# Optimization experiments

Hardware: AMD Instinct MI355X
Metric: run time of the kernel (lower is better)

Reference implementation:

```python
import jax, jax.numpy as jnp
import numpy as np

G = 4        # split_group
H = 64       # hidden_size_t = 256 // 4 (causal -> //1)
I = 64       # input_size_t  = 256 // 4
EPS = 1e-5


def _lstm(x, W_ih, W_hh, b):
    """Grouped unidirectional LSTM, PyTorch gate order (i,f,g,o).
    x: (G,B,T,I); W_ih: (G,4H,I); W_hh: (G,4H,H); b: (G,4H) -> (G,B,T,H)"""
    g, bsz, t, _ = x.shape
    h_dim = W_hh.shape[-1]
    # precompute input projections for all timesteps
    xp = jnp.einsum('gbti,gki->gbtk', x, W_ih) + b[:, None, None, :]  # (G,B,T,4H)
    xp = jnp.moveaxis(xp, 2, 0)  # (T,G,B,4H)

    def step(carry, xt):
        h, c = carry
        gates = xt + jnp.einsum('gbh,gkh->gbk', h, W_hh)
        i_g, f_g, g_g, o_g = jnp.split(gates, 4, axis=-1)
        i_g = jax.nn.sigmoid(i_g)
        f_g = jax.nn.sigmoid(f_g)
        g_g = jnp.tanh(g_g)
        o_g = jax.nn.sigmoid(o_g)
        c = f_g * c + i_g * g_g
        h = o_g * jnp.tanh(c)
        return (h, c), h

    h0 = jnp.zeros((g, bsz, h_dim), x.dtype)
    _, hs = jax.lax.scan(step, (h0, h0), xp)  # hs: (T,G,B,H)
    return jnp.moveaxis(hs, 0, 2)  # (G,B,T,H)


def _bn(x, gamma, beta):
    """BatchNorm1d (training stats) over (B,T) per feature. x: (B,T,F)"""
    mean = x.mean(axis=(0, 1))
    var = x.var(axis=(0, 1))
    return (x - mean) * jax.lax.rsqrt(var + EPS) * gamma + beta


def setup_inputs() -> dict:
    key = jax.random.key(0)
    ks = jax.random.split(key, 12)
    s = 0.1
    F = G * H
    return {
        'inpt': jax.random.normal(ks[0], (32, 1000, 256), jnp.float32),
        'W_ih1': jax.random.normal(ks[1], (G, 4 * H, I), jnp.float32) * s,
        'W_hh1': jax.random.normal(ks[2], (G, 4 * H, H), jnp.float32) * s,
        'b1': jax.random.normal(ks[3], (G, 4 * H), jnp.float32) * s,
        'W_ih2': jax.random.normal(ks[4], (G, 4 * H, H), jnp.float32) * s,
        'W_hh2': jax.random.normal(ks[5], (G, 4 * H, H), jnp.float32) * s,
        'b2': jax.random.normal(ks[6], (G, 4 * H), jnp.float32) * s,
        'gamma1': jnp.ones((F,), jnp.float32) + jax.random.normal(ks[7], (F,)) * 0.01,
        'beta1': jax.random.normal(ks[8], (F,), jnp.float32) * 0.01,
        'gamma2': jnp.ones((F,), jnp.float32) + jax.random.normal(ks[9], (F,)) * 0.01,
        'beta2': jax.random.normal(ks[10], (F,), jnp.float32) * 0.01,
    }


def reference(inpt, W_ih1, W_hh1, b1, W_ih2, W_hh2, b2, gamma1, beta1, gamma2, beta2):
    B, T, F = inpt.shape
    # chunk along features -> (G,B,T,I)
    xg = jnp.transpose(inpt.reshape(B, T, G, I), (2, 0, 1, 3))
    y1 = _lstm(xg, W_ih1, W_hh1, b1)  # (G,B,T,H)
    # torch.stack(dim=-1) + flatten: feature index = h*G + g (interleaved)
    x = jnp.transpose(y1, (1, 2, 3, 0)).reshape(B, T, H * G)
    x = _bn(x, gamma1, beta1)
    # chunk again into G contiguous groups of size H
    xg2 = jnp.transpose(x.reshape(B, T, G, H), (2, 0, 1, 3))
    y2 = _lstm(xg2, W_ih2, W_hh2, b2)  # (G,B,T,H)
    # torch.cat(dim=-1): contiguous groups
    x = jnp.transpose(y2, (1, 2, 0, 3)).reshape(B, T, G * H)
    x = _bn(x, gamma2, beta2)
    return x
```

## Files before the change

kernel.cpp:

```cpp
#include <hip/hip_runtime.h>
#include <math.h>

#define G 4
#define H 64
#define T 1000
#define B 32
#define ROWS (B*T)

__device__ __forceinline__ float sigm(float x) {
    return 1.f / (1.f + __expf(-x));
}
__device__ __forceinline__ float tanh_f(float x) {
    return 2.f / (1.f + __expf(-2.f * x)) - 1.f;
}

template<bool BN>
__global__ __launch_bounds__(256)
void xp_proj(const float* __restrict__ xin,
             const float* __restrict__ Wih,
             const float* __restrict__ bias,
             const float* __restrict__ ac,
             float* __restrict__ xp,
             int t0, int tcn, int tcmax, int TT)
{
    int id = blockIdx.x;
    const int tt = id % TT; id /= TT;
    const int b = id & 31;
    const int g = id >> 5;

    __shared__ __align__(16) float xs[64][68];
    __shared__ __align__(16) float ws[64][68];

    const int tx = threadIdx.x & 15, ty = threadIdx.x >> 4;

    #pragma unroll
    for (int j = 0; j < 4; ++j) {
        int idx = j * 1024 + threadIdx.x * 4;
        int r = idx >> 6, ci = idx & 63;
        int tg = t0 + tt * 64 + r; if (tg > T - 1) tg = T - 1;
        float4 v = *(const float4*)&xin[((size_t)b * T + tg) * 256 + g * 64 + ci];
        if (BN) {
            float4 a4 = *(const float4*)&ac[g * 64 + ci];
            float4 c4 = *(const float4*)&ac[256 + g * 64 + ci];
            v.x = fmaf(v.x, a4.x, c4.x);
            v.y = fmaf(v.y, a4.y, c4.y);
            v.z = fmaf(v.z, a4.z, c4.z);
            v.w = fmaf(v.w, a4.w, c4.w);
        }
        *(float4*)&xs[r][ci] = v;
    }

    float* xpb = xp + (size_t)(g * 32 + b) * tcmax * 256;

    for (int kt = 0; kt < 4; ++kt) {
        __syncthreads();
        #pragma unroll
        for (int j = 0; j < 4; ++j) {
            int idx = j * 1024 + threadIdx.x * 4;
            int r = idx >> 6, ci = idx & 63;
            float4 v = *(const float4*)&Wih[(size_t)((g * 256 + kt * 64 + r) << 6) + ci];
            *(float4*)&ws[r][ci] = v;
        }
        __syncthreads();

        float acc[4][4] = {};
        #pragma unroll
        for (int i4 = 0; i4 < 16; ++i4) {
            float4 xv[4], wv[4];
            #pragma unroll
            for (int q = 0; q < 4; ++q) xv[q] = *(const float4*)&xs[ty * 4 + q][i4 * 4];
            #pragma unroll
            for (int q = 0; q < 4; ++q) wv[q] = *(const float4*)&ws[tx * 4 + q][i4 * 4];
            #pragma unroll
            for (int a = 0; a < 4; ++a)
                #pragma unroll
                for (int c = 0; c < 4; ++c) {
                    acc[a][c] = fmaf(xv[a].x, wv[c].x, acc[a][c]);
                    acc[a][c] = fmaf(xv[a].y, wv[c].y, acc[a][c]);
                    acc[a][c] = fmaf(xv[a].z, wv[c].z, acc[a][c]);
                    acc[a][c] = fmaf(xv[a].w, wv[c].w, acc[a][c]);
                }
        }

        const int kbase = kt * 64 + tx * 4;
        const float4 b4 = *(const float4*)&bias[g * 256 + kbase];
        #pragma unroll
        for (int a = 0; a < 4; ++a) {
            int tloc = tt * 64 + ty * 4 + a;
            if (tloc < tcn) {
                float4 o;
                o.x = acc[a][0] + b4.x;
                o.y = acc[a][1] + b4.y;
                o.z = acc[a][2] + b4.z;
                o.w = acc[a][3] + b4.w;
                *(float4*)&xpb[(size_t)tloc * 256 + kbase] = o;
            }
        }
    }
}

template<int LAYER>
__global__ __launch_bounds__(512, 1)
void rec_xp(const float* __restrict__ xp,
            const float* __restrict__ Whh,
            float* __restrict__ out,
            float* __restrict__ stateh, float* __restrict__ statec,
            float* __restrict__ sums,
            int t0, int t1, int tcmax)
{
    const int blk = blockIdx.x;
    const int g = blk >> 5, b = blk & 31;
    const int tid = threadIdx.x;
    const int w = tid >> 6, l = tid & 63;
    const int c8 = l & 7;
    const int jh = (l >> 3) & 1;
    const int gt = l >> 4;
    const int col = w * 8 + c8;
    const int row = gt * 64 + col;

    __shared__ __align__(16) float hsh[2][64];

    float whh[32];
    {
        const float4* wp = (const float4*)&Whh[(size_t)((g * 256 + row) << 6) + jh * 32];
        #pragma unroll
        for (int i = 0; i < 8; ++i) {
            float4 v = wp[i];
            whh[4*i] = v.x; whh[4*i+1] = v.y; whh[4*i+2] = v.z; whh[4*i+3] = v.w;
        }
    }
    const float m  = (gt == 2) ? 2.f : 1.f;
    const float A  = (gt == 2) ? 2.f : 1.f;
    const float Bc = (gt == 2) ? -1.f : 0.f;

    float cst;
    if (t0 == 0) {
        cst = 0.f;
        if (tid < 64) hsh[0][tid] = 0.f;
    } else {
        cst = statec[blk * 64 + col];
        if (tid < 64) hsh[0][tid] = stateh[blk * 64 + tid];
    }

    const float* xpb = xp + (size_t)blk * tcmax * 256 + row;
    float p[4];
    #pragma unroll
    for (int j = 0; j < 4; ++j) {
        int tp = t0 + j; if (tp > t1 - 1) tp = t1 - 1;
        p[j] = xpb[(size_t)(tp - t0) * 256];
    }

    float hl = 0.f, st_s = 0.f, st_ss = 0.f;
    __syncthreads();

    const int nsteps = t1 - t0;
    for (int s4 = 0; s4 < nsteps; s4 += 4) {
        #pragma unroll
        for (int j = 0; j < 4; ++j) {
            const int cur = j & 1;
            float a0 = 0.f, a1 = 0.f, a2 = 0.f, a3 = 0.f;
            const float4* hv = (const float4*)&hsh[cur][jh * 32];
            #pragma unroll
            for (int q = 0; q < 8; ++q) {
                float4 z = hv[q];
                a0 = fmaf(whh[4*q],   z.x, a0);
                a1 = fmaf(whh[4*q+1], z.y, a1);
                a2 = fmaf(whh[4*q+2], z.z, a2);
                a3 = fmaf(whh[4*q+3], z.w, a3);
            }
            float acc = (a0 + a1) + (a2 + a3);
            float full = acc + __shfl_xor(acc, 8);
            float pre = full + p[j];
            {
                int tp = t0 + s4 + j + 4; if (tp > t1 - 1) tp = t1 - 1;
                p[j] = xpb[(size_t)(tp - t0) * 256];
            }
            float act = A / (1.f + __expf(-m * pre)) + Bc;
            float P = act * __shfl_xor(act, 32);
            float Q = __shfl_xor(P, 16);
            cst = fmaf(act, cst, Q);
            float R = __shfl_xor(cst, 32);
            float h = act * tanh_f(R);
            if (gt == 3 && jh == 0) {
                hsh[cur ^ 1][col] = h;
                int t = t0 + s4 + j;
                if (LAYER == 1) out[((size_t)b * T + t) * 256 + col * 4 + g] = h;
                else            out[((size_t)b * T + t) * 256 + g * 64 + col] = h;
                st_s += h;
                st_ss = fmaf(h, h, st_ss);
                hl = h;
            }
            __syncthreads();
        }
    }
    if (gt == 3 && jh == 0) {
        stateh[blk * 64 + col] = hl;
        int f = (LAYER == 1) ? (col * 4 + g) : (g * 64 + col);
        atomicAdd(&sums[f], st_s);
        atomicAdd(&sums[256 + f], st_ss);
    }
    if (gt == 1 && jh == 0) {
        statec[blk * 64 + col] = cst;
    }
}

template<int LAYER>
__global__ __launch_bounds__(256, 1)
void rec_kernel(const float* __restrict__ xin,
                const float* __restrict__ Wih,
                const float* __restrict__ Whh,
                const float* __restrict__ bias,
                const float* __restrict__ bnac,
                float* __restrict__ out)
{
    const int g = blockIdx.x & 3;
    const int b = blockIdx.x >> 2;
    const int k = threadIdx.x;

    __shared__ __align__(16) float xsh[2][64];
    __shared__ __align__(16) float hsh[64];
    __shared__ __align__(16) float gsh[256];

    float wih[64], whh[64];
    {
        const float4* wi = (const float4*)(Wih + (size_t)(g * 256 + k) * 64);
        const float4* wh = (const float4*)(Whh + (size_t)(g * 256 + k) * 64);
        #pragma unroll
        for (int i = 0; i < 16; ++i) {
            float4 v = wi[i];
            wih[4*i] = v.x; wih[4*i+1] = v.y; wih[4*i+2] = v.z; wih[4*i+3] = v.w;
            float4 u = wh[i];
            whh[4*i] = u.x; whh[4*i+1] = u.y; whh[4*i+2] = u.z; whh[4*i+3] = u.w;
        }
    }
    const float bk = bias[g * 256 + k];
    const long rowbase = (long)b * T;
    const int  colbase = g * 64;

    float c = 0.f, af = 1.f, cf = 0.f;
    float xa = 0.f, xb = 0.f;

    if (k < 64) {
        if (LAYER == 2) { af = bnac[colbase + k]; cf = bnac[256 + colbase + k]; }
        hsh[k] = 0.f;
        float x0 = xin[(rowbase + 0) * 256 + colbase + k];
        xsh[0][k] = (LAYER == 2) ? fmaf(x0, af, cf) : x0;
        xa = xin[(rowbase + 1) * 256 + colbase + k];
        xb = xin[(rowbase + 2) * 256 + colbase + k];
    }
    __syncthreads();

    for (int t = 0; t < T; ++t) {
        const int cur = t & 1;
        float xn = 0.f;
        if (k < 64) {
            int tp = t + 3; if (tp > T - 1) tp = T - 1;
            xn = xin[(rowbase + tp) * 256 + colbase + k];
        }
        const float* xs = xsh[cur];
        float a0 = 0.f, a1 = 0.f, a2 = 0.f, a3 = 0.f;
        #pragma unroll
        for (int i = 0; i < 64; i += 4) {
            a0 = fmaf(wih[i],     xs[i],     a0);
            a1 = fmaf(wih[i + 1], xs[i + 1], a1);
            a2 = fmaf(wih[i + 2], xs[i + 2], a2);
            a3 = fmaf(wih[i + 3], xs[i + 3], a3);
        }
        #pragma unroll
        for (int jq = 0; jq < 64; jq += 4) {
            a0 = fmaf(whh[jq],     hsh[jq],     a0);
            a1 = fmaf(whh[jq + 1], hsh[jq + 1], a1);
            a2 = fmaf(whh[jq + 2], hsh[jq + 2], a2);
            a3 = fmaf(whh[jq + 3], hsh[jq + 3], a3);
        }
        const float acc = bk + ((a0 + a1) + (a2 + a3));
        const float act = (k >= 128 && k < 192) ? tanh_f(acc) : sigm(acc);
        gsh[k] = act;
        __syncthreads();

        if (k < 64) {
            const float ig = gsh[k];
            const float fg = gsh[64 + k];
            const float gg = gsh[128 + k];
            const float og = gsh[192 + k];
            c = fmaf(fg, c, ig * gg);
            const float h = og * tanh_f(c);
            hsh[k] = h;
            const long rrow = rowbase + t;
            if (LAYER == 1) out[rrow * 256 + k * 4 + g] = h;
            else            out[rrow * 256 + colbase + k] = h;
            xsh[cur ^ 1][k] = fmaf(xa, af, cf);
            xa = xb; xb = xn;
        }
        __syncthreads();
    }
}

__global__ void zero_ws(float* sums, int n) {
    int i = blockIdx.x * blockDim.x + threadIdx.x;
    if (i < n) sums[i] = 0.f;
}

__global__ __launch_bounds__(256) void stats_reduce(const float* __restrict__ x,
                                                    float* __restrict__ sums)
{
    float s = 0.f, ss = 0.f;
    for (int r = blockIdx.x; r < ROWS; r += gridDim.x) {
        float v = x[(long)r * 256 + threadIdx.x];
        s += v;
        ss = fmaf(v, v, ss);
    }
    atomicAdd(&sums[threadIdx.x], s);
    atomicAdd(&sums[256 + threadIdx.x], ss);
}

__global__ void stats_finalize(const float* __restrict__ sums,
                               const float* __restrict__ gamma,
                               const float* __restrict__ beta,
                               float* __restrict__ ac)
{
    int f = threadIdx.x;
    const float invN = 1.f / (float)ROWS;
    float mean = sums[f] * invN;
    float var  = fmaf(-mean, mean, sums[256 + f] * invN);
    float a = gamma[f] * rsqrtf(var + 1e-5f);
    ac[f]       = a;
    ac[256 + f] = fmaf(-mean, a, beta[f]);
}

__global__ __launch_bounds__(256) void bn_apply(float* __restrict__ x,
                                                const float* __restrict__ ac)
{
    __shared__ float a_s[256], c_s[256];
    a_s[threadIdx.x] = ac[threadIdx.x];
    c_s[threadIdx.x] = ac[256 + threadIdx.x];
    __syncthreads();
    const long n4 = (long)ROWS * 64;
    for (long i = (long)blockIdx.x * blockDim.x + threadIdx.x; i < n4;
         i += (long)gridDim.x * blockDim.x) {
        float4 v = ((float4*)x)[i];
        int f0 = (int)((i * 4) & 255);
        v.x = fmaf(v.x, a_s[f0],     c_s[f0]);
        v.y = fmaf(v.y, a_s[f0 + 1], c_s[f0 + 1]);
        v.z = fmaf(v.z, a_s[f0 + 2], c_s[f0 + 2]);
        v.w = fmaf(v.w, a_s[f0 + 3], c_s[f0 + 3]);
        ((float4*)x)[i] = v;
    }
}

extern "C" void kernel_launch(void* const* d_in, const int* in_sizes, int n_in,
                              void* d_out, int out_size, void* d_ws, size_t ws_size,
                              hipStream_t stream)
{
    const float* inpt   = (const float*)d_in[0];
    const float* Wih1   = (const float*)d_in[1];
    const float* Whh1   = (const float*)d_in[2];
    const float* b1     = (const float*)d_in[3];
    const float* Wih2   = (const float*)d_in[4];
    const float* Whh2   = (const float*)d_in[5];
    const float* b2     = (const float*)d_in[6];
    const float* gamma1 = (const float*)d_in[7];
    const float* beta1  = (const float*)d_in[8];
    const float* gamma2 = (const float*)d_in[9];
    const float* beta2  = (const float*)d_in[10];
    float* out  = (float*)d_out;

    float* sums1 = (float*)d_ws;
    float* sums2 = sums1 + 512;
    float* acbn1 = sums2 + 512;
    float* acbn2 = acbn1 + 512;
    float* sth   = acbn2 + 512;
    float* stc   = sth + 8192;
    float* xpb   = stc + 8192;

    const size_t fixedB = (size_t)(4 * 512 + 2 * 8192) * 4;
    long availT = ((long)ws_size - (long)fixedB) / (128L * 256L * 4L);
    int Tcmax = (availT >= T) ? T : (int)(availT & ~3L);

    if (Tcmax >= 100) {
        zero_ws<<<4, 256, 0, stream>>>(sums1, 1024);

        for (int t0 = 0; t0 < T; t0 += Tcmax) {
            int tcn = T - t0; if (tcn > Tcmax) tcn = Tcmax;
            int TT = (tcn + 63) / 64;
            xp_proj<false><<<128 * TT, 256, 0, stream>>>(
                inpt, Wih1, b1, nullptr, xpb, t0, tcn, Tcmax, TT);
            rec_xp<1><<<128, 512, 0, stream>>>(xpb, Whh1, out, sth, stc, sums1,
                                               t0, t0 + tcn, Tcmax);
        }
        stats_finalize<<<1, 256, 0, stream>>>(sums1, gamma1, beta1, acbn1);

        for (int t0 = 0; t0 < T; t0 += Tcmax) {
            int tcn = T - t0; if (tcn > Tcmax) tcn = Tcmax;
            int TT = (tcn + 63) / 64;
            xp_proj<true><<<128 * TT, 256, 0, stream>>>(
                out, Wih2, b2, acbn1, xpb, t0, tcn, Tcmax, TT);
            rec_xp<2><<<128, 512, 0, stream>>>(xpb, Whh2, out, sth, stc, sums2,
                                               t0, t0 + tcn, Tcmax);
        }
        stats_finalize<<<1, 256, 0, stream>>>(sums2, gamma2, beta2, acbn2);
        bn_apply<<<2048, 256, 0, stream>>>(out, acbn2);
    } else {
        zero_ws<<<2, 256, 0, stream>>>(sums1, 512);
        rec_kernel<1><<<G * B, 256, 0, stream>>>(inpt, Wih1, Whh1, b1, nullptr, out);
        stats_reduce<<<256, 256, 0, stream>>>(out, sums1);
        stats_finalize<<<1, 256, 0, stream>>>(sums1, gamma1, beta1, acbn1);
        rec_kernel<2><<<G * B, 256, 0, stream>>>(out, Wih2, Whh2, b2, acbn1, out);
        zero_ws<<<2, 256, 0, stream>>>(sums2, 512);
        stats_reduce<<<256, 256, 0, stream>>>(out, sums2);
        stats_finalize<<<1, 256, 0, stream>>>(sums2, gamma2, beta2, acbn2);
        bn_apply<<<2048, 256, 0, stream>>>(out, acbn2);
    }
}
```

Baseline: 1.536 ms.

## Overlap input projection with recurrence via double-buffered fused chunk kernels

Splits the time axis into chunks and double-buffers the input-projection workspace, so one fused launch runs the recurrence on the current chunk while extra blocks compute the projection for the next chunk. The recurrent kernel also drops from 512 to 256 threads: each thread now holds a full 64-element W_hh row, which removes the split-K shuffle and simplifies the gate exchange. A lighter workgroup barrier and a raised wave priority are added. The costs are higher register pressure, more sequential FMAs per thread, and projection blocks competing for CUs with the latency-bound recurrence. If the workspace is small the chunks become shorter.

```diff
diff --git a/kernel.cpp b/kernel.cpp
--- a/kernel.cpp
+++ b/kernel.cpp
@@ -14,22 +14,27 @@
     return 2.f / (1.f + __expf(-2.f * x)) - 1.f;
 }
 
+__device__ __forceinline__ void wg_barrier() {
+    asm volatile("s_waitcnt lgkmcnt(0)" ::: "memory");
+    __builtin_amdgcn_s_barrier();
+    __builtin_amdgcn_sched_barrier(0);
+}
+
 template<bool BN>
-__global__ __launch_bounds__(256)
-void xp_proj(const float* __restrict__ xin,
+__device__ __forceinline__ void proj_body(int id,
+             const float* __restrict__ xin,
              const float* __restrict__ Wih,
              const float* __restrict__ bias,
              const float* __restrict__ ac,
              float* __restrict__ xp,
              int t0, int tcn, int tcmax, int TT)
 {
-    int id = blockIdx.x;
     const int tt = id % TT; id /= TT;
     const int b = id & 31;
     const int g = id >> 5;
 
     __shared__ __align__(16) float xs[64][68];
-    __shared__ __align__(16) float ws[64][68];
+    __shared__ __align__(16) float wsm[64][68];
 
     const int tx = threadIdx.x & 15, ty = threadIdx.x >> 4;
 
@@ -59,7 +64,7 @@
             int idx = j * 1024 + threadIdx.x * 4;
             int r = idx >> 6, ci = idx & 63;
             float4 v = *(const float4*)&Wih[(size_t)((g * 256 + kt * 64 + r) << 6) + ci];
-            *(float4*)&ws[r][ci] = v;
+            *(float4*)&wsm[r][ci] = v;
         }
         __syncthreads();
 
@@ -70,7 +75,7 @@
             #pragma unroll
             for (int q = 0; q < 4; ++q) xv[q] = *(const float4*)&xs[ty * 4 + q][i4 * 4];
             #pragma unroll
-            for (int q = 0; q < 4; ++q) wv[q] = *(const float4*)&ws[tx * 4 + q][i4 * 4];
+            for (int q = 0; q < 4; ++q) wv[q] = *(const float4*)&wsm[tx * 4 + q][i4 * 4];
             #pragma unroll
             for (int a = 0; a < 4; ++a)
                 #pragma unroll
@@ -99,32 +104,39 @@
     }
 }
 
+template<bool BN>
+__global__ __launch_bounds__(256)
+void xp_proj(const float* __restrict__ xin, const float* __restrict__ Wih,
+             const float* __restrict__ bias, const float* __restrict__ ac,
+             float* __restrict__ xp, int t0, int tcn, int tcmax, int TT)
+{
+    proj_body<BN>(blockIdx.x, xin, Wih, bias, ac, xp, t0, tcn, tcmax, TT);
+}
+
 template<int LAYER>
-__global__ __launch_bounds__(512, 1)
-void rec_xp(const float* __restrict__ xp,
+__device__ __forceinline__ void rec_body(
+            const float* __restrict__ xp,
             const float* __restrict__ Whh,
             float* __restrict__ out,
             float* __restrict__ stateh, float* __restrict__ statec,
             float* __restrict__ sums,
             int t0, int t1, int tcmax)
 {
+    __builtin_amdgcn_s_setprio(1);
     const int blk = blockIdx.x;
     const int g = blk >> 5, b = blk & 31;
-    const int tid = threadIdx.x;
-    const int w = tid >> 6, l = tid & 63;
-    const int c8 = l & 7;
-    const int jh = (l >> 3) & 1;
-    const int gt = l >> 4;
-    const int col = w * 8 + c8;
+    const int l = threadIdx.x & 63, w = threadIdx.x >> 6;
+    const int c16 = l & 15, gt = l >> 4;
+    const int col = w * 16 + c16;
     const int row = gt * 64 + col;
 
     __shared__ __align__(16) float hsh[2][64];
 
-    float whh[32];
+    float whh[64];
     {
-        const float4* wp = (const float4*)&Whh[(size_t)((g * 256 + row) << 6) + jh * 32];
-        #pragma unroll
-        for (int i = 0; i < 8; ++i) {
+        const float4* wp = (const float4*)&Whh[(size_t)((g * 256 + row) << 6)];
+        #pragma unroll
+        for (int i = 0; i < 16; ++i) {
             float4 v = wp[i];
             whh[4*i] = v.x; whh[4*i+1] = v.y; whh[4*i+2] = v.z; whh[4*i+3] = v.w;
         }
@@ -133,13 +145,12 @@
     const float A  = (gt == 2) ? 2.f : 1.f;
     const float Bc = (gt == 2) ? -1.f : 0.f;
 
-    float cst;
+    float cst = 0.f;
     if (t0 == 0) {
-        cst = 0.f;
-        if (tid < 64) hsh[0][tid] = 0.f;
+        if (threadIdx.x < 64) hsh[0][threadIdx.x] = 0.f;
     } else {
         cst = statec[blk * 64 + col];
-        if (tid < 64) hsh[0][tid] = stateh[blk * 64 + tid];
+        if (threadIdx.x < 64) hsh[0][threadIdx.x] = stateh[blk * 64 + threadIdx.x];
     }
 
     const float* xpb = xp + (size_t)blk * tcmax * 256 + row;
@@ -159,29 +170,27 @@
         for (int j = 0; j < 4; ++j) {
             const int cur = j & 1;
             float a0 = 0.f, a1 = 0.f, a2 = 0.f, a3 = 0.f;
-            const float4* hv = (const float4*)&hsh[cur][jh * 32];
+            const float4* hv = (const float4*)hsh[cur];
             #pragma unroll
-            for (int q = 0; q < 8; ++q) {
+            for (int q = 0; q < 16; ++q) {
                 float4 z = hv[q];
                 a0 = fmaf(whh[4*q],   z.x, a0);
                 a1 = fmaf(whh[4*q+1], z.y, a1);
                 a2 = fmaf(whh[4*q+2], z.z, a2);
                 a3 = fmaf(whh[4*q+3], z.w, a3);
             }
-            float acc = (a0 + a1) + (a2 + a3);
-            float full = acc + __shfl_xor(acc, 8);
-            float pre = full + p[j];
+            float pre = ((a0 + a1) + (a2 + a3)) + p[j];
             {
                 int tp = t0 + s4 + j + 4; if (tp > t1 - 1) tp = t1 - 1;
                 p[j] = xpb[(size_t)(tp - t0) * 256];
             }
             float act = A / (1.f + __expf(-m * pre)) + Bc;
-            float P = act * __shfl_xor(act, 32);
-            float Q = __shfl_xor(P, 16);
-            cst = fmaf(act, cst, Q);
-            float R = __shfl_xor(cst, 32);
-            float h = act * tanh_f(R);
-            if (gt == 3 && jh == 0) {
+            float gg = __shfl_xor(act, 16);
+            float fg = __shfl_xor(act, 32);
+            float ig = __shfl_xor(act, 48);
+            cst = fmaf(fg, cst, ig * gg);
+            float h = act * tanh_f(cst);
+            if (gt == 3) {
                 hsh[cur ^ 1][col] = h;
                 int t = t0 + s4 + j;
                 if (LAYER == 1) out[((size_t)b * T + t) * 256 + col * 4 + g] = h;
@@ -190,17 +199,34 @@
                 st_ss = fmaf(h, h, st_ss);
                 hl = h;
             }
-            __syncthreads();
-        }
-    }
-    if (gt == 3 && jh == 0) {
+            wg_barrier();
+        }
+    }
+    if (gt == 3) {
         stateh[blk * 64 + col] = hl;
+        statec[blk * 64 + col] = cst;
         int f = (LAYER == 1) ? (col * 4 + g) : (g * 64 + col);
         atomicAdd(&sums[f], st_s);
         atomicAdd(&sums[256 + f], st_ss);
     }
-    if (gt == 1 && jh == 0) {
-        statec[blk * 64 + col] = cst;
+}
+
+template<int LAYER, bool PBN>
+__global__ __launch_bounds__(256, 1)
+void fused_step(const float* __restrict__ xpA, const float* __restrict__ Whh,
+                float* __restrict__ out,
+                float* __restrict__ stateh, float* __restrict__ statec,
+                float* __restrict__ sums,
+                int t0, int t1, int tcmax,
+                const float* __restrict__ xin, const float* __restrict__ Wih,
+                const float* __restrict__ bias, const float* __restrict__ acbn,
+                float* __restrict__ xpB, int t0n, int tcnn, int TTn)
+{
+    if (blockIdx.x < 128) {
+        rec_body<LAYER>(xpA, Whh, out, stateh, statec, sums, t0, t1, tcmax);
+    } else {
+        proj_body<PBN>(blockIdx.x - 128, xin, Wih, bias, acbn, xpB,
+                       t0n, tcnn, tcmax, TTn);
     }
 }
 
@@ -374,29 +400,48 @@
     float* xpb   = stc + 8192;
 
     const size_t fixedB = (size_t)(4 * 512 + 2 * 8192) * 4;
-    long availT = ((long)ws_size - (long)fixedB) / (128L * 256L * 4L);
-    int Tcmax = (availT >= T) ? T : (int)(availT & ~3L);
-
-    if (Tcmax >= 100) {
+    const long perT = 128L * 256L * 4L;
+    long availPair = ((long)ws_size - (long)fixedB) / (2L * perT);
+    int Tc = (availPair >= T) ? T : (int)(availPair & ~3L);
+
+    if (Tc >= 8) {
+        float* buf[2] = { xpb, xpb + (size_t)Tc * 128 * 256 };
+        const int nch = (T + Tc - 1) / Tc;
         zero_ws<<<4, 256, 0, stream>>>(sums1, 1024);
 
-        for (int t0 = 0; t0 < T; t0 += Tcmax) {
-            int tcn = T - t0; if (tcn > Tcmax) tcn = Tcmax;
-            int TT = (tcn + 63) / 64;
-            xp_proj<false><<<128 * TT, 256, 0, stream>>>(
-                inpt, Wih1, b1, nullptr, xpb, t0, tcn, Tcmax, TT);
-            rec_xp<1><<<128, 512, 0, stream>>>(xpb, Whh1, out, sth, stc, sums1,
-                                               t0, t0 + tcn, Tcmax);
+        {
+            int tcn0 = (Tc < T) ? Tc : T;
+            int TT0 = (tcn0 + 63) / 64;
+            xp_proj<false><<<128 * TT0, 256, 0, stream>>>(
+                inpt, Wih1, b1, nullptr, buf[0], 0, tcn0, Tc, TT0);
+            for (int c = 0; c < nch; ++c) {
+                int t0 = c * Tc;
+                int t1 = t0 + Tc; if (t1 > T) t1 = T;
+                int t0n = t1;
+                int tcnn = (c + 1 < nch) ? ((T - t0n < Tc) ? (T - t0n) : Tc) : 0;
+                int TTn = (tcnn + 63) / 64;
+                fused_step<1, false><<<128 + 128 * TTn, 256, 0, stream>>>(
+                    buf[c & 1], Whh1, out, sth, stc, sums1, t0, t1, Tc,
+                    inpt, Wih1, b1, nullptr, buf[(c + 1) & 1], t0n, tcnn, TTn);
+            }
         }
         stats_finalize<<<1, 256, 0, stream>>>(sums1, gamma1, beta1, acbn1);
 
-        for (int t0 = 0; t0 < T; t0 += Tcmax) {
-            int tcn = T - t0; if (tcn > Tcmax) tcn = Tcmax;
-            int TT = (tcn + 63) / 64;
-            xp_proj<true><<<128 * TT, 256, 0, stream>>>(
-                out, Wih2, b2, acbn1, xpb, t0, tcn, Tcmax, TT);
-            rec_xp<2><<<128, 512, 0, stream>>>(xpb, Whh2, out, sth, stc, sums2,
-                                               t0, t0 + tcn, Tcmax);
+        {
+            int tcn0 = (Tc < T) ? Tc : T;
+            int TT0 = (tcn0 + 63) / 64;
+            xp_proj<true><<<128 * TT0, 256, 0, stream>>>(
+                out, Wih2, b2, acbn1, buf[0], 0, tcn0, Tc, TT0);
+            for (int c = 0; c < nch; ++c) {
+                int t0 = c * Tc;
+                int t1 = t0 + Tc; if (t1 > T) t1 = T;
+                int t0n = t1;
+                int tcnn = (c + 1 < nch) ? ((T - t0n < Tc) ? (T - t0n) : Tc) : 0;
+                int TTn = (tcnn + 63) / 64;
+                fused_step<2, true><<<128 + 128 * TTn, 256, 0, stream>>>(
+                    buf[c & 1], Whh2, out, sth, stc, sums2, t0, t1, Tc,
+                    out, Wih2, b2, acbn1, buf[(c + 1) & 1], t0n, tcnn, TTn);
+            }
         }
         stats_finalize<<<1, 256, 0, stream>>>(sums2, gamma2, beta2, acbn2);
         bn_apply<<<2048, 256, 0, stream>>>(out, acbn2);
```

New measurement: 1.583 ms. 1.03x slower.

## Pack two sequences per block with all-four-gate threads in recurrent kernel

Applied to the files above, without the earlier changes.

The recurrent LSTM kernel now runs two (group,batch) sequences per 512-thread block, using 256 threads per sequence. Each thread holds all four gate rows for one hidden column over a 16-wide k slice and reduces across lanes with two xor shuffles. This removes the cross-gate shuffles and halves the number of blocks. The plain __syncthreads is replaced by a custom barrier that waits on LDS and sets wave priority. The cost is longer per-thread FMA chains and the two sequences stepping in lockstep under one barrier.

```diff
diff --git a/kernel.cpp b/kernel.cpp
--- a/kernel.cpp
+++ b/kernel.cpp
@@ -12,6 +12,12 @@
 }
 __device__ __forceinline__ float tanh_f(float x) {
     return 2.f / (1.f + __expf(-2.f * x)) - 1.f;
+}
+
+__device__ __forceinline__ void wg_barrier() {
+    asm volatile("s_waitcnt lgkmcnt(0)" ::: "memory");
+    __builtin_amdgcn_s_barrier();
+    __builtin_amdgcn_sched_barrier(0);
 }
 
 template<bool BN>
@@ -29,7 +35,7 @@
     const int g = id >> 5;
 
     __shared__ __align__(16) float xs[64][68];
-    __shared__ __align__(16) float ws[64][68];
+    __shared__ __align__(16) float wsm[64][68];
 
     const int tx = threadIdx.x & 15, ty = threadIdx.x >> 4;
 
@@ -59,7 +65,7 @@
             int idx = j * 1024 + threadIdx.x * 4;
             int r = idx >> 6, ci = idx & 63;
             float4 v = *(const float4*)&Wih[(size_t)((g * 256 + kt * 64 + r) << 6) + ci];
-            *(float4*)&ws[r][ci] = v;
+            *(float4*)&wsm[r][ci] = v;
         }
         __syncthreads();
 
@@ -70,7 +76,7 @@
             #pragma unroll
             for (int q = 0; q < 4; ++q) xv[q] = *(const float4*)&xs[ty * 4 + q][i4 * 4];
             #pragma unroll
-            for (int q = 0; q < 4; ++q) wv[q] = *(const float4*)&ws[tx * 4 + q][i4 * 4];
+            for (int q = 0; q < 4; ++q) wv[q] = *(const float4*)&wsm[tx * 4 + q][i4 * 4];
             #pragma unroll
             for (int a = 0; a < 4; ++a)
                 #pragma unroll
@@ -101,53 +107,52 @@
 
 template<int LAYER>
 __global__ __launch_bounds__(512, 1)
-void rec_xp(const float* __restrict__ xp,
-            const float* __restrict__ Whh,
-            float* __restrict__ out,
-            float* __restrict__ stateh, float* __restrict__ statec,
-            float* __restrict__ sums,
-            int t0, int t1, int tcmax)
-{
-    const int blk = blockIdx.x;
+void rec2(const float* __restrict__ xp,
+          const float* __restrict__ Whh,
+          float* __restrict__ out,
+          float* __restrict__ stateh, float* __restrict__ statec,
+          float* __restrict__ sums,
+          int t0, int t1, int tcmax)
+{
+    __builtin_amdgcn_s_setprio(1);
+    const int seq = threadIdx.x >> 8;
+    const int tid = threadIdx.x & 255;
+    const int blk = blockIdx.x * 2 + seq;
     const int g = blk >> 5, b = blk & 31;
-    const int tid = threadIdx.x;
     const int w = tid >> 6, l = tid & 63;
-    const int c8 = l & 7;
-    const int jh = (l >> 3) & 1;
-    const int gt = l >> 4;
-    const int col = w * 8 + c8;
-    const int row = gt * 64 + col;
-
-    __shared__ __align__(16) float hsh[2][64];
-
-    float whh[32];
-    {
-        const float4* wp = (const float4*)&Whh[(size_t)((g * 256 + row) << 6) + jh * 32];
-        #pragma unroll
-        for (int i = 0; i < 8; ++i) {
-            float4 v = wp[i];
-            whh[4*i] = v.x; whh[4*i+1] = v.y; whh[4*i+2] = v.z; whh[4*i+3] = v.w;
-        }
-    }
-    const float m  = (gt == 2) ? 2.f : 1.f;
-    const float A  = (gt == 2) ? 2.f : 1.f;
-    const float Bc = (gt == 2) ? -1.f : 0.f;
-
-    float cst;
+    const int c16 = l & 15, ks = l >> 4;
+    const int col = w * 16 + c16;
+
+    __shared__ __align__(16) float hsh[2][2][64];
+
+    float whh[4][16];
+    #pragma unroll
+    for (int gt = 0; gt < 4; ++gt) {
+        const float4* wp = (const float4*)&Whh[(size_t)((g * 256 + gt * 64 + col) << 6) + ks * 16];
+        #pragma unroll
+        for (int q = 0; q < 4; ++q) {
+            float4 v = wp[q];
+            whh[gt][q*4+0] = v.x; whh[gt][q*4+1] = v.y;
+            whh[gt][q*4+2] = v.z; whh[gt][q*4+3] = v.w;
+        }
+    }
+
+    float cst = 0.f;
     if (t0 == 0) {
-        cst = 0.f;
-        if (tid < 64) hsh[0][tid] = 0.f;
+        if (tid < 64) hsh[seq][0][tid] = 0.f;
     } else {
         cst = statec[blk * 64 + col];
-        if (tid < 64) hsh[0][tid] = stateh[blk * 64 + tid];
-    }
-
-    const float* xpb = xp + (size_t)blk * tcmax * 256 + row;
-    float p[4];
+        if (tid < 64) hsh[seq][0][tid] = stateh[blk * 64 + tid];
+    }
+
+    const float* xpb = xp + (size_t)blk * tcmax * 256;
+    float p[4][4];
     #pragma unroll
     for (int j = 0; j < 4; ++j) {
         int tp = t0 + j; if (tp > t1 - 1) tp = t1 - 1;
-        p[j] = xpb[(size_t)(tp - t0) * 256];
+        #pragma unroll
+        for (int gt = 0; gt < 4; ++gt)
+            p[j][gt] = xpb[(size_t)(tp - t0) * 256 + gt * 64 + col];
     }
 
     float hl = 0.f, st_s = 0.f, st_ss = 0.f;
@@ -158,31 +163,46 @@
         #pragma unroll
         for (int j = 0; j < 4; ++j) {
             const int cur = j & 1;
-            float a0 = 0.f, a1 = 0.f, a2 = 0.f, a3 = 0.f;
-            const float4* hv = (const float4*)&hsh[cur][jh * 32];
+            float4 hv[4];
             #pragma unroll
-            for (int q = 0; q < 8; ++q) {
-                float4 z = hv[q];
-                a0 = fmaf(whh[4*q],   z.x, a0);
-                a1 = fmaf(whh[4*q+1], z.y, a1);
-                a2 = fmaf(whh[4*q+2], z.z, a2);
-                a3 = fmaf(whh[4*q+3], z.w, a3);
+            for (int q = 0; q < 4; ++q)
+                hv[q] = *(const float4*)&hsh[seq][cur][ks * 16 + q * 4];
+
+            float pre[4];
+            #pragma unroll
+            for (int gt = 0; gt < 4; ++gt) {
+                float a0 = 0.f, a1 = 0.f;
+                #pragma unroll
+                for (int q = 0; q < 4; q += 2) {
+                    float4 z0 = hv[q], z1 = hv[q + 1];
+                    a0 = fmaf(whh[gt][q*4+0],     z0.x, a0);
+                    a0 = fmaf(whh[gt][q*4+1],     z0.y, a0);
+                    a0 = fmaf(whh[gt][q*4+2],     z0.z, a0);
+                    a0 = fmaf(whh[gt][q*4+3],     z0.w, a0);
+                    a1 = fmaf(whh[gt][(q+1)*4+0], z1.x, a1);
+                    a1 = fmaf(whh[gt][(q+1)*4+1], z1.y, a1);
+                    a1 = fmaf(whh[gt][(q+1)*4+2], z1.z, a1);
+                    a1 = fmaf(whh[gt][(q+1)*4+3], z1.w, a1);
+                }
+                float v = a0 + a1;
+                v += __shfl_xor(v, 16);
+                v += __shfl_xor(v, 32);
+                pre[gt] = v + p[j][gt];
             }
-            float acc = (a0 + a1) + (a2 + a3);
-            float full = acc + __shfl_xor(acc, 8);
-            float pre = full + p[j];
             {
                 int tp = t0 + s4 + j + 4; if (tp > t1 - 1) tp = t1 - 1;
-                p[j] = xpb[(size_t)(tp - t0) * 256];
+                #pragma unroll
+                for (int gt = 0; gt < 4; ++gt)
+                    p[j][gt] = xpb[(size_t)(tp - t0) * 256 + gt * 64 + col];
             }
-            float act = A / (1.f + __expf(-m * pre)) + Bc;
-            float P = act * __shfl_xor(act, 32);
-            float Q = __shfl_xor(P, 16);
-            cst = fmaf(act, cst, Q);
-            float R = __shfl_xor(cst, 32);
-            float h = act * tanh_f(R);
-            if (gt == 3 && jh == 0) {
-                hsh[cur ^ 1][col] = h;
+            float ig = sigm(pre[0]);
+            float fg = sigm(pre[1]);
+            float gg = tanh_f(pre[2]);
+            float og = sigm(pre[3]);
+            cst = fmaf(fg, cst, ig * gg);
+            float h = og * tanh_f(cst);
+            if (l < 16) {
+                hsh[seq][cur ^ 1][col] = h;
                 int t = t0 + s4 + j;
                 if (LAYER == 1) out[((size_t)b * T + t) * 256 + col * 4 + g] = h;
                 else            out[((size_t)b * T + t) * 256 + g * 64 + col] = h;
@@ -190,17 +210,15 @@
                 st_ss = fmaf(h, h, st_ss);
                 hl = h;
             }
-            __syncthreads();
-        }
-    }
-    if (gt == 3 && jh == 0) {
+            wg_barrier();
+        }
+    }
+    if (l < 16) {
         stateh[blk * 64 + col] = hl;
+        statec[blk * 64 + col] = cst;
         int f = (LAYER == 1) ? (col * 4 + g) : (g * 64 + col);
         atomicAdd(&sums[f], st_s);
         atomicAdd(&sums[256 + f], st_ss);
-    }
-    if (gt == 1 && jh == 0) {
-        statec[blk * 64 + col] = cst;
     }
 }
 
@@ -374,29 +392,30 @@
     float* xpb   = stc + 8192;
 
     const size_t fixedB = (size_t)(4 * 512 + 2 * 8192) * 4;
-    long availT = ((long)ws_size - (long)fixedB) / (128L * 256L * 4L);
-    int Tcmax = (availT >= T) ? T : (int)(availT & ~3L);
-
-    if (Tcmax >= 100) {
+    const long perT = 128L * 256L * 4L;
+    long availT = ((long)ws_size - (long)fixedB) / perT;
+    int Tc = (availT >= T) ? T : (int)(availT & ~3L);
+
+    if (Tc >= 8) {
         zero_ws<<<4, 256, 0, stream>>>(sums1, 1024);
 
-        for (int t0 = 0; t0 < T; t0 += Tcmax) {
-            int tcn = T - t0; if (tcn > Tcmax) tcn = Tcmax;
+        for (int t0 = 0; t0 < T; t0 += Tc) {
+            int tcn = T - t0; if (tcn > Tc) tcn = Tc;
             int TT = (tcn + 63) / 64;
             xp_proj<false><<<128 * TT, 256, 0, stream>>>(
-                inpt, Wih1, b1, nullptr, xpb, t0, tcn, Tcmax, TT);
-            rec_xp<1><<<128, 512, 0, stream>>>(xpb, Whh1, out, sth, stc, sums1,
-                                               t0, t0 + tcn, Tcmax);
+                inpt, Wih1, b1, nullptr, xpb, t0, tcn, Tc, TT);
+            rec2<1><<<64, 512, 0, stream>>>(xpb, Whh1, out, sth, stc, sums1,
+                                            t0, t0 + tcn, Tc);
         }
         stats_finalize<<<1, 256, 0, stream>>>(sums1, gamma1, beta1, acbn1);
 
-        for (int t0 = 0; t0 < T; t0 += Tcmax) {
-            int tcn = T - t0; if (tcn > Tcmax) tcn = Tcmax;
+        for (int t0 = 0; t0 < T; t0 += Tc) {
+            int tcn = T - t0; if (tcn > Tc) tcn = Tc;
             int TT = (tcn + 63) / 64;
             xp_proj<true><<<128 * TT, 256, 0, stream>>>(
-                out, Wih2, b2, acbn1, xpb, t0, tcn, Tcmax, TT);
-            rec_xp<2><<<128, 512, 0, stream>>>(xpb, Whh2, out, sth, stc, sums2,
-                                               t0, t0 + tcn, Tcmax);
+                out, Wih2, b2, acbn1, xpb, t0, tcn, Tc, TT);
+            rec2<2><<<64, 512, 0, stream>>>(xpb, Whh2, out, sth, stc, sums2,
+                                            t0, t0 + tcn, Tc);
         }
         stats_finalize<<<1, 256, 0, stream>>>(sums2, gamma2, beta2, acbn2);
         bn_apply<<<2048, 256, 0, stream>>>(out, acbn2);
```

After: 1.957 ms. +27.4%, slower.
